# Kernel tuning notes

Hardware: AMD Instinct MI355X
Metric: run time of the kernel (lower is better)

The kernel has to match this reference:

```python
import jax, jax.numpy as jnp
import numpy as np

F, H, S, B, T = 1024, 512, 512, 32, 128  # feat_size, hid_size, seq_len, batch, max_out_len


def setup_inputs() -> dict:
    key = jax.random.key(0)
    ks = jax.random.split(key, 20)
    sc = 0.05
    def p(k, shape):
        return jax.random.normal(k, shape, dtype=jnp.float32) * sc
    return {
        "feats": jax.random.normal(ks[0], (S, B, F), dtype=jnp.float32),
        # encoder forward-direction LSTM (PyTorch gate order i,f,g,o)
        "Wih_f": p(ks[1], (4 * H, F)), "Whh_f": p(ks[2], (4 * H, H)),
        "bih_f": p(ks[3], (4 * H,)), "bhh_f": p(ks[4], (4 * H,)),
        # encoder backward-direction LSTM
        "Wih_b": p(ks[5], (4 * H, F)), "Whh_b": p(ks[6], (4 * H, H)),
        "bih_b": p(ks[7], (4 * H,)), "bhh_b": p(ks[8], (4 * H,)),
        # decoder LSTMCell(F -> 2H)
        "Wih_d": p(ks[9], (8 * H, F)), "Whh_d": p(ks[10], (8 * H, 2 * H)),
        "bih_d": p(ks[11], (8 * H,)), "bhh_d": p(ks[12], (8 * H,)),
        # attention projections
        "W_enc": p(ks[13], (H, 2 * H)), "b_enc": p(ks[14], (H,)),
        "W_dec": p(ks[15], (H, 2 * H)), "b_dec": p(ks[16], (H,)),
        "W_v": p(ks[17], (1, H)), "b_v": p(ks[18], (1,)),
    }


def _cell(x, h, c, Wih, Whh, bih, bhh):
    g = x @ Wih.T + h @ Whh.T + bih + bhh
    i, f, gg, o = jnp.split(g, 4, axis=-1)
    c = jax.nn.sigmoid(f) * c + jax.nn.sigmoid(i) * jnp.tanh(gg)
    return jax.nn.sigmoid(o) * jnp.tanh(c), c


def _run_lstm(seq, Wih, Whh, bih, bhh, hid):
    b = seq.shape[1]
    init = (jnp.zeros((b, hid), seq.dtype), jnp.zeros((b, hid), seq.dtype))
    def step(carry, x):
        h, c = _cell(x, carry[0], carry[1], Wih, Whh, bih, bhh)
        return (h, c), h
    (h, c), hs = jax.lax.scan(step, init, seq)
    return hs, h, c


def reference(feats, Wih_f, Whh_f, bih_f, bhh_f, Wih_b, Whh_b, bih_b, bhh_b,
              Wih_d, Whh_d, bih_d, bhh_d, W_enc, b_enc, W_dec, b_dec, W_v, b_v):
    s, b, _ = feats.shape
    hs_f, hf, cf = _run_lstm(feats, Wih_f, Whh_f, bih_f, bhh_f, H)
    hs_b, hb, cb = _run_lstm(feats[::-1], Wih_b, Whh_b, bih_b, bhh_b, H)
    enc_out = jnp.concatenate([hs_f, hs_b[::-1]], axis=-1)  # [S,B,2H]
    # torch h.view((B, -1)) on [2,B,H] is a raw reshape, reproduced exactly
    h0 = jnp.stack([hf, hb]).reshape(b, 2 * H)
    c0 = jnp.stack([cf, cb]).reshape(b, 2 * H)
    enc_proj = enc_out @ W_enc.T + b_enc  # [S,B,H], hoisted out of the step loop
    bidx = jnp.arange(b)

    def dec_step(carry, _):
        h, c, inp = carry
        h, c = _cell(inp, h, c, Wih_d, Whh_d, bih_d, bhh_d)
        dproj = h @ W_dec.T + b_dec  # [B,H]
        scores = (jnp.tanh(enc_proj + dproj[None]) @ W_v.T + b_v)[..., 0].T  # [B,S]
        idx = jnp.argmax(scores, axis=1)  # greedy pointer (is_train=False path)
        nxt = feats[idx, bidx]  # [B,F]
        return (h, c, nxt), scores

    _, ys = jax.lax.scan(dec_step, (h0, c0, feats[0]), None, length=T)  # [T,B,S]
    return ys.reshape(T * b, s)
```

## Files before the change

kernel.cpp:

```cpp
#include <hip/hip_runtime.h>
#include <stdint.h>


#define NWG 256

__device__ __forceinline__ float sigm(float x) { return 1.0f / (1.0f + __expf(-x)); }
__device__ __forceinline__ float tanhx(float x) {
  float e = __expf(2.0f * x);
  return 1.0f - 2.0f / (e + 1.0f);
}

__device__ __forceinline__ float ldc(const float* p) {
  return __hip_atomic_load(p, __ATOMIC_RELAXED, __HIP_MEMORY_SCOPE_AGENT);
}
__device__ __forceinline__ float2 ldc2(const float* p) {
  double d = __hip_atomic_load((const double*)p, __ATOMIC_RELAXED, __HIP_MEMORY_SCOPE_AGENT);
  return __builtin_bit_cast(float2, d);
}
__device__ __forceinline__ void stc(float* p, float v) {
  __hip_atomic_store(p, v, __ATOMIC_RELAXED, __HIP_MEMORY_SCOPE_AGENT);
}
__device__ __forceinline__ int ldci(const int* p) {
  return __hip_atomic_load(p, __ATOMIC_RELAXED, __HIP_MEMORY_SCOPE_AGENT);
}
__device__ __forceinline__ void stci(int* p, int v) {
  __hip_atomic_store(p, v, __ATOMIC_RELAXED, __HIP_MEMORY_SCOPE_AGENT);
}

__device__ __forceinline__ void tree_barrier(int* bar, int w, int epoch) {
  __syncthreads();
  if (threadIdx.x == 0) {
    const int g = w >> 3;
    int* gc = bar + g * 64;
    int* rc = bar + 2048;
    int* gf = bar + 2112 + g * 64;
    int old = __hip_atomic_fetch_add(gc, 1, __ATOMIC_RELAXED, __HIP_MEMORY_SCOPE_AGENT);
    if (old == epoch * 8 - 1) {
      __hip_atomic_fetch_add(rc, 1, __ATOMIC_RELAXED, __HIP_MEMORY_SCOPE_AGENT);
      while (__hip_atomic_load(rc, __ATOMIC_RELAXED, __HIP_MEMORY_SCOPE_AGENT) < epoch * 32)
        __builtin_amdgcn_s_sleep(2);
      __hip_atomic_store(gf, epoch, __ATOMIC_RELAXED, __HIP_MEMORY_SCOPE_AGENT);
    } else {
      while (__hip_atomic_load(gf, __ATOMIC_RELAXED, __HIP_MEMORY_SCOPE_AGENT) < epoch)
        __builtin_amdgcn_s_sleep(2);
    }
  }
  __syncthreads();
}

__global__ __launch_bounds__(256) void xproj_gemm(
    const float* __restrict__ A, const float* __restrict__ W,
    float* __restrict__ C)
{
  __shared__ float As[16][68];
  __shared__ float Ws[16][68];
  const int t = threadIdx.x;
  const int m0 = blockIdx.x * 64, n0 = blockIdx.y * 64;
  const int tx = t & 15, ty = t >> 4;
  const int lr = t >> 2, lk = (t & 3) * 4;
  float acc[4][4] = {{0.f}};

  for (int kb = 0; kb < 1024; kb += 16) {
    float4 a4 = *(const float4*)(A + (size_t)(m0 + lr) * 1024 + kb + lk);
    float4 w4 = *(const float4*)(W + (size_t)(n0 + lr) * 1024 + kb + lk);
    __syncthreads();
    As[lk + 0][lr] = a4.x; As[lk + 1][lr] = a4.y;
    As[lk + 2][lr] = a4.z; As[lk + 3][lr] = a4.w;
    Ws[lk + 0][lr] = w4.x; Ws[lk + 1][lr] = w4.y;
    Ws[lk + 2][lr] = w4.z; Ws[lk + 3][lr] = w4.w;
    __syncthreads();
#pragma unroll
    for (int kk = 0; kk < 16; ++kk) {
      float4 av = *(const float4*)(&As[kk][ty * 4]);
      float4 wv = *(const float4*)(&Ws[kk][tx * 4]);
      acc[0][0] += av.x * wv.x; acc[0][1] += av.x * wv.y;
      acc[0][2] += av.x * wv.z; acc[0][3] += av.x * wv.w;
      acc[1][0] += av.y * wv.x; acc[1][1] += av.y * wv.y;
      acc[1][2] += av.y * wv.z; acc[1][3] += av.y * wv.w;
      acc[2][0] += av.z * wv.x; acc[2][1] += av.z * wv.y;
      acc[2][2] += av.z * wv.z; acc[2][3] += av.z * wv.w;
      acc[3][0] += av.w * wv.x; acc[3][1] += av.w * wv.y;
      acc[3][2] += av.w * wv.z; acc[3][3] += av.w * wv.w;
    }
  }
#pragma unroll
  for (int i = 0; i < 4; ++i) {
    float4 o;
    o.x = acc[i][0]; o.y = acc[i][1]; o.z = acc[i][2]; o.w = acc[i][3];
    *(float4*)(C + (size_t)(m0 + ty * 4 + i) * 2048 + n0 + tx * 4) = o;
  }
}

__global__ __launch_bounds__(512) void encoder_kernel(
    const float* __restrict__ feats,
    const float* __restrict__ Wih_f, const float* __restrict__ Whh_f,
    const float* __restrict__ bih_f, const float* __restrict__ bhh_f,
    const float* __restrict__ Wih_b, const float* __restrict__ Whh_b,
    const float* __restrict__ bih_b, const float* __restrict__ bhh_b,
    const float* __restrict__ W_enc, const float* __restrict__ b_enc,
    const float* __restrict__ xg_f, const float* __restrict__ xg_b,
    float* __restrict__ enc_proj, float* __restrict__ henc,
    float* __restrict__ cfin, int* __restrict__ bar)
{
  extern __shared__ __align__(16) float dyn[];
  float* wih_l = dyn;
  float* whh_l = dyn + 16448;
  __shared__ float hch[32 * 132];
  __shared__ float wenc[4 * 516];
  __shared__ float gpart[32][17];
  __shared__ float projp[2][128];
  __shared__ float bias_s[16];
  __shared__ float benc_s[4];

  const int w = blockIdx.x;
  const int dir = (w >= 128) ? 1 : 0;
  const int wl = w & 127;
  const int col0 = wl * 4;
  const int t = threadIdx.x;
  const int g = t >> 7;
  const int tt = t & 127;
  const int b = tt >> 2;
  const int ci = tt & 3;
  const int col = col0 + ci;
  const int i0 = t, i1 = t + 512;
  const int bb0 = i0 >> 5, q0 = i0 & 31;
  const int bb1 = i1 >> 5, q1 = i1 & 31;

  const float* Wih = dir ? Wih_b : Wih_f;
  const float* Whh = dir ? Whh_b : Whh_f;
  const float* bih = dir ? bih_b : bih_f;
  const float* bhh = dir ? bhh_b : bhh_f;
  const float* xg  = dir ? xg_b : xg_f;

  if (!xg) {
    for (int i = t; i < 16 * 256; i += 512) {
      int r = i >> 8, q = i & 255;
      int gg = r >> 2, cj = r & 3;
      *(float4*)(wih_l + r * 1028 + q * 4) =
          *(const float4*)(Wih + (size_t)(gg * 512 + col0 + cj) * 1024 + q * 4);
    }
  }
  for (int i = t; i < 16 * 128; i += 512) {
    int r = i >> 7, q = i & 127;
    int gg = r >> 2, cj = r & 3;
    *(float4*)(whh_l + r * 516 + q * 4) =
        *(const float4*)(Whh + (size_t)(gg * 512 + col0 + cj) * 512 + q * 4);
  }
  for (int i = t; i < 4 * 128; i += 512) {
    int jl = i >> 7, q = i & 127;
    *(float4*)(wenc + jl * 516 + q * 4) =
        *(const float4*)(W_enc + (size_t)(col0 + jl) * 1024 + dir * 512 + q * 4);
  }
  if (t < 16) {
    int gg = t >> 2, cj = t & 3;
    bias_s[t] = bih[gg * 512 + col0 + cj] + bhh[gg * 512 + col0 + cj];
  }
  if (t < 4) benc_s[t] = b_enc[col0 + t];
  float c_reg = 0.0f;
  __syncthreads();

  const float* wx = wih_l + (g * 4 + ci) * 1028;
  const float* wh = whh_l + (g * 4 + ci) * 516;
  const float* wpe = wenc + ci * 516;
  const size_t xg_row = (size_t)(g * 512 + col);

  for (int it = 0; it < 512; ++it) {
    const int s = dir ? (511 - it) : it;
    float acc = 0.0f, projacc = 0.0f;
    float xgv = 0.0f;
    if (xg) xgv = xg[(size_t)(s * 32 + b) * 2048 + xg_row];

    if (it > 0) {
      const float* hsrc = henc + dir * 32768 + ((it - 1) & 1) * 16384;
      float2 rA0, rA1, rB0, rB1;
      rA0 = ldc2(hsrc + bb0 * 512 + q0 * 4);
      rA1 = ldc2(hsrc + bb0 * 512 + q0 * 4 + 2);
      rB0 = ldc2(hsrc + bb1 * 512 + q1 * 4);
      rB1 = ldc2(hsrc + bb1 * 512 + q1 * 4 + 2);
      for (int ch = 0; ch < 4; ++ch) {
        *(float4*)(hch + bb0 * 132 + q0 * 4) = make_float4(rA0.x, rA0.y, rA1.x, rA1.y);
        *(float4*)(hch + bb1 * 132 + q1 * 4) = make_float4(rB0.x, rB0.y, rB1.x, rB1.y);
        __syncthreads();
        if (ch < 3) {
          rA0 = ldc2(hsrc + bb0 * 512 + (ch + 1) * 128 + q0 * 4);
          rA1 = ldc2(hsrc + bb0 * 512 + (ch + 1) * 128 + q0 * 4 + 2);
          rB0 = ldc2(hsrc + bb1 * 512 + (ch + 1) * 128 + q1 * 4);
          rB1 = ldc2(hsrc + bb1 * 512 + (ch + 1) * 128 + q1 * 4 + 2);
        }
        {
          const float* hrow = hch + b * 132;
          const float* p0 = wh + ch * 128;
#pragma unroll 8
          for (int q = 0; q < 32; ++q) {
            float4 h4 = *(const float4*)(hrow + q * 4);
            float4 a4 = *(const float4*)(p0 + q * 4);
            acc += h4.x * a4.x + h4.y * a4.y + h4.z * a4.z + h4.w * a4.w;
          }
        }
        if (g < 2) {
          const float* hp = hch + b * 132 + g * 64;
          const float* wp = wpe + ch * 128 + g * 64;
#pragma unroll 4
          for (int kk = 0; kk < 16; ++kk) {
            float4 h4 = *(const float4*)(hp + kk * 4);
            float4 w4 = *(const float4*)(wp + kk * 4);
            projacc += h4.x * w4.x + h4.y * w4.y + h4.z * w4.z + h4.w * w4.w;
          }
        }
        __syncthreads();
      }
    }

    if (!xg) {
      const float* fsrc = feats + ((size_t)s * 32) * 1024;
      float4 fA = *(const float4*)(fsrc + bb0 * 1024 + q0 * 4);
      float4 fB = *(const float4*)(fsrc + bb1 * 1024 + q1 * 4);
      for (int ch = 0; ch < 8; ++ch) {
        *(float4*)(hch + bb0 * 132 + q0 * 4) = fA;
        *(float4*)(hch + bb1 * 132 + q1 * 4) = fB;
        __syncthreads();
        if (ch < 7) {
          fA = *(const float4*)(fsrc + bb0 * 1024 + (ch + 1) * 128 + q0 * 4);
          fB = *(const float4*)(fsrc + bb1 * 1024 + (ch + 1) * 128 + q1 * 4);
        }
        const float* hrow = hch + b * 132;
        const float* p0 = wx + ch * 128;
#pragma unroll 8
        for (int q = 0; q < 32; ++q) {
          float4 f4 = *(const float4*)(hrow + q * 4);
          float4 a4 = *(const float4*)(p0 + q * 4);
          acc += f4.x * a4.x + f4.y * a4.y + f4.z * a4.z + f4.w * a4.w;
        }
        __syncthreads();
      }
    }

    gpart[b][g * 4 + ci] = acc + xgv;
    if (g < 2) projp[g][tt] = projacc;
    __syncthreads();
    if (t < 128) {
      float gi = gpart[b][ci + 0] + bias_s[ci + 0];
      float gf = gpart[b][ci + 4] + bias_s[ci + 4];
      float gg = gpart[b][ci + 8] + bias_s[ci + 8];
      float go = gpart[b][ci + 12] + bias_s[ci + 12];
      float cn = sigm(gf) * c_reg + sigm(gi) * tanhx(gg);
      c_reg = cn;
      stc(henc + dir * 32768 + (it & 1) * 16384 + b * 512 + col,
          sigm(go) * tanhx(cn));
    } else if (g == 1 && it > 0) {
      const int sp = dir ? (512 - it) : (it - 1);
      const float p = projp[0][tt] + projp[1][tt];
      float* addr = enc_proj + ((size_t)sp * 32 + b) * 512 + col;
      if (it - 1 <= 255) {
        stc(addr, p + benc_s[ci]);
      } else {
        stc(addr, ldc(addr) + p);
      }
    }
    tree_barrier(bar, w, it + 1);
  }

  {
    const float* hsrc = henc + dir * 32768 + 16384;
    float projacc = 0.0f;
    for (int ch = 0; ch < 4; ++ch) {
      for (int i = t; i < 1024; i += 512) {
        int bb = i >> 5, q = i & 31;
        const float* sp = hsrc + bb * 512 + ch * 128 + q * 4;
        float2 f0 = ldc2(sp);
        float2 f1 = ldc2(sp + 2);
        *(float4*)(hch + bb * 132 + q * 4) = make_float4(f0.x, f0.y, f1.x, f1.y);
      }
      __syncthreads();
      if (g < 2) {
        const float* hp = hch + b * 132 + g * 64;
        const float* wp = wpe + ch * 128 + g * 64;
#pragma unroll 4
        for (int kk = 0; kk < 16; ++kk) {
          float4 h4 = *(const float4*)(hp + kk * 4);
          float4 w4 = *(const float4*)(wp + kk * 4);
          projacc += h4.x * w4.x + h4.y * w4.y + h4.z * w4.z + h4.w * w4.w;
        }
      }
      __syncthreads();
    }
    if (g < 2) projp[g][tt] = projacc;
    __syncthreads();
    if (g == 1) {
      const int sp = dir ? 0 : 511;
      float* addr = enc_proj + ((size_t)sp * 32 + b) * 512 + col;
      stc(addr, ldc(addr) + (projp[0][tt] + projp[1][tt]));
    }
    if (t < 128) cfin[dir * 16384 + b * 512 + col] = c_reg;
  }
}

__global__ __launch_bounds__(512) void decoder_kernel(
    const float* __restrict__ feats,
    const float* __restrict__ Wih_d, const float* __restrict__ Whh_d,
    const float* __restrict__ bih_d, const float* __restrict__ bhh_d,
    const float* __restrict__ W_dec, const float* __restrict__ b_dec,
    const float* __restrict__ W_v, const float* __restrict__ b_v,
    const float* __restrict__ enc_proj, const float* __restrict__ henc,
    const float* __restrict__ cfin,
    float* __restrict__ hbuf, float* __restrict__ dproj,
    float* __restrict__ pval, int* __restrict__ pidx,
    int* __restrict__ bar, float* __restrict__ out)
{
  extern __shared__ __align__(16) float dyn[];
  float* whh_l = dyn;
  float* wih_l = dyn + 16448;
  __shared__ float hch[32 * 132];
  __shared__ float gpart[2][32][17];
  __shared__ float c_lds[32][4];
  __shared__ float bias_s[16];
  __shared__ float svals[64];
  __shared__ int ib_lds[32];
  float* dpl = hch + 1088;

  const int w = blockIdx.x;
  const int t = threadIdx.x;
  const int q4 = t >> 7;
  const int tt = t & 127;
  const int b = tt >> 2;
  const int ci = tt & 3;
  const int col0 = w * 4;
  const int col = col0 + ci;
  const int i0 = t, i1 = t + 512;
  const int bb0 = i0 >> 5, q0 = i0 & 31;
  const int bb1 = i1 >> 5, q1 = i1 & 31;
  const int bb_c = w >> 3;
  const int qq_ = w & 7;
  const int ccB = t >> 8;
  const int bB = (t >> 3) & 31;
  const int k8 = t & 7;

  for (int i = t; i < 16 * 256; i += 512) {
    int r = i >> 8, q = i & 255;
    int gg = r >> 2, cj = r & 3;
    *(float4*)(whh_l + r * 1028 + q * 4) =
        *(const float4*)(Whh_d + (size_t)(gg * 1024 + col0 + cj) * 1024 + q * 4);
    *(float4*)(wih_l + r * 1028 + q * 4) =
        *(const float4*)(Wih_d + (size_t)(gg * 1024 + col0 + cj) * 1024 + q * 4);
  }
  if (t < 16) {
    int gg = t >> 2, cj = t & 3;
    bias_s[t] = bih_d[gg * 1024 + col0 + cj] + bhh_d[gg * 1024 + col0 + cj];
  }
  if (t < 128) {
    int flat = b * 1024 + col;
    int d = flat >> 14, sb = (flat >> 9) & 31, sh = flat & 511;
    float h0, c0;
    if (d == 0) {
      h0 = henc[16384 + sb * 512 + sh];
      c0 = cfin[sb * 512 + sh];
    } else {
      h0 = henc[32768 + 16384 + sb * 512 + sh];
      c0 = cfin[16384 + sb * 512 + sh];
    }
    stc(hbuf + b * 1024 + col, h0);
    c_lds[b][ci] = c0;
  }
  int bars = 1;
  tree_barrier(bar, w, bars);

  const float* wbase = (q4 < 2) ? whh_l : wih_l;
  const int g0 = (q4 & 1) * 2;
  const float* wr0 = wbase + (size_t)((g0 + 0) * 4 + ci) * 1028;
  const float* wr1 = wbase + (size_t)((g0 + 1) * 4 + ci) * 1028;

  for (int ts = 0; ts < 128; ++ts) {
    const float* hprev = hbuf + (ts & 1) * 32768;
    float* hnext = hbuf + ((ts + 1) & 1) * 32768;

    float a0 = 0.f, a1 = 0.f;
    const float* xrow = nullptr;
    {
      float2 rA0 = ldc2(hprev + bb0 * 1024 + q0 * 4);
      float2 rA1 = ldc2(hprev + bb0 * 1024 + q0 * 4 + 2);
      float2 rB0 = ldc2(hprev + bb1 * 1024 + q1 * 4);
      float2 rB1 = ldc2(hprev + bb1 * 1024 + q1 * 4 + 2);
      if (t < 32) {
        int ib = 0;
        if (ts > 0) {
          float v = ldc(pval + t * 8 + 0);
          int si = ldci(pidx + t * 8 + 0);
#pragma unroll
          for (int j = 1; j < 8; ++j) {
            float ov = ldc(pval + t * 8 + j);
            int os = ldci(pidx + t * 8 + j);
            if (ov > v || (ov == v && os < si)) { v = ov; si = os; }
          }
          ib = si;
        }
        ib_lds[t] = ib;
      }
      for (int ch = 0; ch < 8; ++ch) {
        *(float4*)(hch + bb0 * 132 + q0 * 4) = make_float4(rA0.x, rA0.y, rA1.x, rA1.y);
        *(float4*)(hch + bb1 * 132 + q1 * 4) = make_float4(rB0.x, rB0.y, rB1.x, rB1.y);
        __syncthreads();
        if (ch == 0 && q4 >= 2) {
          int ib = ib_lds[b];
          xrow = feats + ((size_t)ib * 32 + b) * 1024;
        }
        if (ch < 7) {
          rA0 = ldc2(hprev + bb0 * 1024 + (ch + 1) * 128 + q0 * 4);
          rA1 = ldc2(hprev + bb0 * 1024 + (ch + 1) * 128 + q0 * 4 + 2);
          rB0 = ldc2(hprev + bb1 * 1024 + (ch + 1) * 128 + q1 * 4);
          rB1 = ldc2(hprev + bb1 * 1024 + (ch + 1) * 128 + q1 * 4 + 2);
        }
        const float* src = (q4 < 2) ? (hch + b * 132) : (xrow + ch * 128);
        const float* p0 = wr0 + ch * 128;
        const float* p1 = wr1 + ch * 128;
#pragma unroll 8
        for (int qq = 0; qq < 32; ++qq) {
          float4 h4 = *(const float4*)(src + qq * 4);
          float4 u0 = *(const float4*)(p0 + qq * 4);
          float4 u1 = *(const float4*)(p1 + qq * 4);
          a0 += h4.x * u0.x + h4.y * u0.y + h4.z * u0.z + h4.w * u0.w;
          a1 += h4.x * u1.x + h4.y * u1.y + h4.z * u1.z + h4.w * u1.w;
        }
        __syncthreads();
      }
    }
    gpart[q4 >> 1][b][ci + (g0 + 0) * 4] = a0;
    gpart[q4 >> 1][b][ci + (g0 + 1) * 4] = a1;
    __syncthreads();
    if (t < 128) {
      float gi = gpart[0][b][ci + 0] + gpart[1][b][ci + 0] + bias_s[ci + 0];
      float gf = gpart[0][b][ci + 4] + gpart[1][b][ci + 4] + bias_s[ci + 4];
      float gg = gpart[0][b][ci + 8] + gpart[1][b][ci + 8] + bias_s[ci + 8];
      float go = gpart[0][b][ci + 12] + gpart[1][b][ci + 12] + bias_s[ci + 12];
      float cn = sigm(gf) * c_lds[b][ci] + sigm(gi) * tanhx(gg);
      c_lds[b][ci] = cn;
      stc(hnext + b * 1024 + col, sigm(go) * tanhx(cn));
    }
    ++bars; tree_barrier(bar, w, bars);

    {
      float dacc = 0.f;
      const float* wdrow = W_dec + (size_t)(2 * w + ccB) * 1024;
      float2 rA0 = ldc2(hnext + bb0 * 1024 + q0 * 4);
      float2 rA1 = ldc2(hnext + bb0 * 1024 + q0 * 4 + 2);
      float2 rB0 = ldc2(hnext + bb1 * 1024 + q1 * 4);
      float2 rB1 = ldc2(hnext + bb1 * 1024 + q1 * 4 + 2);
      for (int ch = 0; ch < 8; ++ch) {
        *(float4*)(hch + bb0 * 132 + q0 * 4) = make_float4(rA0.x, rA0.y, rA1.x, rA1.y);
        *(float4*)(hch + bb1 * 132 + q1 * 4) = make_float4(rB0.x, rB0.y, rB1.x, rB1.y);
        __syncthreads();
        if (ch < 7) {
          rA0 = ldc2(hnext + bb0 * 1024 + (ch + 1) * 128 + q0 * 4);
          rA1 = ldc2(hnext + bb0 * 1024 + (ch + 1) * 128 + q0 * 4 + 2);
          rB0 = ldc2(hnext + bb1 * 1024 + (ch + 1) * 128 + q1 * 4);
          rB1 = ldc2(hnext + bb1 * 1024 + (ch + 1) * 128 + q1 * 4 + 2);
        }
        const float* hl = hch + bB * 132 + k8 * 16;
        const float* wl = wdrow + ch * 128 + k8 * 16;
#pragma unroll
        for (int j = 0; j < 4; ++j) {
          float4 h4 = *(const float4*)(hl + j * 4);
          float4 w4 = *(const float4*)(wl + j * 4);
          dacc += h4.x * w4.x + h4.y * w4.y + h4.z * w4.z + h4.w * w4.w;
        }
        __syncthreads();
      }
      dacc += __shfl_xor(dacc, 1);
      dacc += __shfl_xor(dacc, 2);
      dacc += __shfl_xor(dacc, 4);
      if (k8 == 0) stc(dproj + bB * 512 + 2 * w + ccB, dacc + b_dec[2 * w + ccB]);
    }
    ++bars; tree_barrier(bar, w, bars);

    if (t < 256) {
      float2 v = ldc2(dproj + bb_c * 512 + 2 * t);
      int k = 2 * t;
      dpl[(k >> 6) * 68 + (k & 63) + 0] = v.x;
      dpl[(k >> 6) * 68 + (k & 63) + 1] = v.y;
    }
    __syncthreads();
    {
      const int sl = t >> 3, ks = t & 7;
      const int s = qq_ * 64 + sl;
      const float* ep = enc_proj + ((size_t)s * 32 + bb_c) * 512 + ks * 64;
      const float* dpp = dpl + ks * 68;
      const float* wvp = W_v + ks * 64;
      float sum = 0.f;
#pragma unroll 4
      for (int j = 0; j < 16; ++j) {
        float4 e4 = *(const float4*)(ep + j * 4);
        float4 d4 = *(const float4*)(dpp + j * 4);
        float4 v4 = *(const float4*)(wvp + j * 4);
        sum += tanhx(e4.x + d4.x) * v4.x;
        sum += tanhx(e4.y + d4.y) * v4.y;
        sum += tanhx(e4.z + d4.z) * v4.z;
        sum += tanhx(e4.w + d4.w) * v4.w;
      }
      sum += __shfl_xor(sum, 1);
      sum += __shfl_xor(sum, 2);
      sum += __shfl_xor(sum, 4);
      if (ks == 0) {
        float sv = sum + b_v[0];
        out[((size_t)ts * 32 + bb_c) * 512 + s] = sv;
        svals[sl] = sv;
      }
    }
    __syncthreads();
    if (t < 64) {
      float v = svals[t];
      int si = qq_ * 64 + t;
#pragma unroll
      for (int m = 1; m < 64; m <<= 1) {
        float ov = __shfl_xor(v, m);
        int os = __shfl_xor(si, m);
        if (ov > v || (ov == v && os < si)) { v = ov; si = os; }
      }
      if (t == 0) {
        stc(pval + bb_c * 8 + qq_, v);
        stci(pidx + bb_c * 8 + qq_, si);
      }
    }
    ++bars; tree_barrier(bar, w, bars);
  }
}

extern "C" void kernel_launch(void* const* d_in, const int* in_sizes, int n_in,
                              void* d_out, int out_size, void* d_ws, size_t ws_size,
                              hipStream_t stream) {
  (void)in_sizes; (void)n_in; (void)out_size;
  const float* feats = (const float*)d_in[0];
  const float* Wih_f = (const float*)d_in[1];
  const float* Whh_f = (const float*)d_in[2];
  const float* bih_f = (const float*)d_in[3];
  const float* bhh_f = (const float*)d_in[4];
  const float* Wih_b = (const float*)d_in[5];
  const float* Whh_b = (const float*)d_in[6];
  const float* bih_b = (const float*)d_in[7];
  const float* bhh_b = (const float*)d_in[8];
  const float* Wih_d = (const float*)d_in[9];
  const float* Whh_d = (const float*)d_in[10];
  const float* bih_d = (const float*)d_in[11];
  const float* bhh_d = (const float*)d_in[12];
  const float* W_enc = (const float*)d_in[13];
  const float* b_enc = (const float*)d_in[14];
  const float* W_dec = (const float*)d_in[15];
  const float* b_dec = (const float*)d_in[16];
  const float* W_v   = (const float*)d_in[17];
  const float* b_v   = (const float*)d_in[18];
  float* out = (float*)d_out;

  int* ctrl = (int*)d_ws;
  int* bar_enc = ctrl;
  int* bar_dec = ctrl + 8192;
  float* base = (float*)d_ws + 16384;
  float* enc_proj = base;
  float* henc     = enc_proj + 8388608;
  float* cfin     = henc + 65536;
  float* hbuf     = cfin + 32768;
  float* dproj    = hbuf + 65536;
  float* pval     = dproj + 16384;
  int*   pidx     = (int*)(pval + 8192);
  float* xg_base  = pval + 16384;

  const size_t xg_elems = (size_t)16384 * 2048;
  const size_t need_xg_bytes =
      (size_t)(16384 + 8388608 + 65536 + 32768 + 65536 + 16384 + 16384) * 4 +
      2 * xg_elems * 4 + (1 << 20);
  const bool use_xg = ws_size >= need_xg_bytes;
  const float* xg_f = use_xg ? xg_base : nullptr;
  const float* xg_b = use_xg ? (xg_base + xg_elems) : nullptr;

  const int ENC_LDS = (16 * 1028 + 16 * 516) * 4;
  const int DEC_LDS = (2 * 16 * 1028) * 4;
  hipFuncSetAttribute((const void*)encoder_kernel,
                      hipFuncAttributeMaxDynamicSharedMemorySize, ENC_LDS);
  hipFuncSetAttribute((const void*)decoder_kernel,
                      hipFuncAttributeMaxDynamicSharedMemorySize, DEC_LDS);

  hipMemsetAsync(d_ws, 0, 65536, stream);

  if (use_xg) {
    dim3 gg(256, 32);
    xproj_gemm<<<gg, 256, 0, stream>>>(feats, Wih_f, (float*)xg_f);
    xproj_gemm<<<gg, 256, 0, stream>>>(feats, Wih_b, (float*)xg_b);
  }

  {
    void* args[] = {(void*)&feats,
                    (void*)&Wih_f, (void*)&Whh_f, (void*)&bih_f, (void*)&bhh_f,
                    (void*)&Wih_b, (void*)&Whh_b, (void*)&bih_b, (void*)&bhh_b,
                    (void*)&W_enc, (void*)&b_enc, (void*)&xg_f, (void*)&xg_b,
                    (void*)&enc_proj, (void*)&henc, (void*)&cfin, (void*)&bar_enc};
    hipLaunchCooperativeKernel((const void*)encoder_kernel, dim3(NWG), dim3(512),
                               args, ENC_LDS, stream);
  }
  {
    void* args[] = {(void*)&feats,
                    (void*)&Wih_d, (void*)&Whh_d, (void*)&bih_d, (void*)&bhh_d,
                    (void*)&W_dec, (void*)&b_dec, (void*)&W_v, (void*)&b_v,
                    (void*)&enc_proj, (void*)&henc, (void*)&cfin,
                    (void*)&hbuf, (void*)&dproj, (void*)&pval, (void*)&pidx,
                    (void*)&bar_dec, (void*)&out};
    hipLaunchCooperativeKernel((const void*)decoder_kernel, dim3(NWG), dim3(512),
                               args, DEC_LDS, stream);
  }
}
```

Measured before the change: 19.38 ms.

## Drop precomputed input-projection GEMM and fuse x-projection into encoder recurrence

```diff
diff --git a/kernel.cpp b/kernel.cpp
--- a/kernel.cpp
+++ b/kernel.cpp
@@ -48,49 +48,6 @@
   __syncthreads();
 }
 
-__global__ __launch_bounds__(256) void xproj_gemm(
-    const float* __restrict__ A, const float* __restrict__ W,
-    float* __restrict__ C)
-{
-  __shared__ float As[16][68];
-  __shared__ float Ws[16][68];
-  const int t = threadIdx.x;
-  const int m0 = blockIdx.x * 64, n0 = blockIdx.y * 64;
-  const int tx = t & 15, ty = t >> 4;
-  const int lr = t >> 2, lk = (t & 3) * 4;
-  float acc[4][4] = {{0.f}};
-
-  for (int kb = 0; kb < 1024; kb += 16) {
-    float4 a4 = *(const float4*)(A + (size_t)(m0 + lr) * 1024 + kb + lk);
-    float4 w4 = *(const float4*)(W + (size_t)(n0 + lr) * 1024 + kb + lk);
-    __syncthreads();
-    As[lk + 0][lr] = a4.x; As[lk + 1][lr] = a4.y;
-    As[lk + 2][lr] = a4.z; As[lk + 3][lr] = a4.w;
-    Ws[lk + 0][lr] = w4.x; Ws[lk + 1][lr] = w4.y;
-    Ws[lk + 2][lr] = w4.z; Ws[lk + 3][lr] = w4.w;
-    __syncthreads();
-#pragma unroll
-    for (int kk = 0; kk < 16; ++kk) {
-      float4 av = *(const float4*)(&As[kk][ty * 4]);
-      float4 wv = *(const float4*)(&Ws[kk][tx * 4]);
-      acc[0][0] += av.x * wv.x; acc[0][1] += av.x * wv.y;
-      acc[0][2] += av.x * wv.z; acc[0][3] += av.x * wv.w;
-      acc[1][0] += av.y * wv.x; acc[1][1] += av.y * wv.y;
-      acc[1][2] += av.y * wv.z; acc[1][3] += av.y * wv.w;
-      acc[2][0] += av.z * wv.x; acc[2][1] += av.z * wv.y;
-      acc[2][2] += av.z * wv.z; acc[2][3] += av.z * wv.w;
-      acc[3][0] += av.w * wv.x; acc[3][1] += av.w * wv.y;
-      acc[3][2] += av.w * wv.z; acc[3][3] += av.w * wv.w;
-    }
-  }
-#pragma unroll
-  for (int i = 0; i < 4; ++i) {
-    float4 o;
-    o.x = acc[i][0]; o.y = acc[i][1]; o.z = acc[i][2]; o.w = acc[i][3];
-    *(float4*)(C + (size_t)(m0 + ty * 4 + i) * 2048 + n0 + tx * 4) = o;
-  }
-}
-
 __global__ __launch_bounds__(512) void encoder_kernel(
     const float* __restrict__ feats,
     const float* __restrict__ Wih_f, const float* __restrict__ Whh_f,
@@ -98,14 +55,13 @@
     const float* __restrict__ Wih_b, const float* __restrict__ Whh_b,
     const float* __restrict__ bih_b, const float* __restrict__ bhh_b,
     const float* __restrict__ W_enc, const float* __restrict__ b_enc,
-    const float* __restrict__ xg_f, const float* __restrict__ xg_b,
     float* __restrict__ enc_proj, float* __restrict__ henc,
     float* __restrict__ cfin, int* __restrict__ bar)
 {
   extern __shared__ __align__(16) float dyn[];
   float* wih_l = dyn;
   float* whh_l = dyn + 16448;
-  __shared__ float hch[32 * 132];
+  __shared__ float hch[32 * 260];
   __shared__ float wenc[4 * 516];
   __shared__ float gpart[32][17];
   __shared__ float projp[2][128];
@@ -122,23 +78,21 @@
   const int b = tt >> 2;
   const int ci = tt & 3;
   const int col = col0 + ci;
-  const int i0 = t, i1 = t + 512;
-  const int bb0 = i0 >> 5, q0 = i0 & 31;
-  const int bb1 = i1 >> 5, q1 = i1 & 31;
+  const int p0i = t,        p0b = p0i >> 6, p0q = p0i & 63;
+  const int p1i = t + 512,  p1b = p1i >> 6, p1q = p1i & 63;
+  const int p2i = t + 1024, p2b = p2i >> 6, p2q = p2i & 63;
+  const int p3i = t + 1536, p3b = p3i >> 6, p3q = p3i & 63;
 
   const float* Wih = dir ? Wih_b : Wih_f;
   const float* Whh = dir ? Whh_b : Whh_f;
   const float* bih = dir ? bih_b : bih_f;
   const float* bhh = dir ? bhh_b : bhh_f;
-  const float* xg  = dir ? xg_b : xg_f;
-
-  if (!xg) {
-    for (int i = t; i < 16 * 256; i += 512) {
-      int r = i >> 8, q = i & 255;
-      int gg = r >> 2, cj = r & 3;
-      *(float4*)(wih_l + r * 1028 + q * 4) =
-          *(const float4*)(Wih + (size_t)(gg * 512 + col0 + cj) * 1024 + q * 4);
-    }
+
+  for (int i = t; i < 16 * 256; i += 512) {
+    int r = i >> 8, q = i & 255;
+    int gg = r >> 2, cj = r & 3;
+    *(float4*)(wih_l + r * 1028 + q * 4) =
+        *(const float4*)(Wih + (size_t)(gg * 512 + col0 + cj) * 1024 + q * 4);
   }
   for (int i = t; i < 16 * 128; i += 512) {
     int r = i >> 7, q = i & 127;
@@ -162,80 +116,112 @@
   const float* wx = wih_l + (g * 4 + ci) * 1028;
   const float* wh = whh_l + (g * 4 + ci) * 516;
   const float* wpe = wenc + ci * 516;
-  const size_t xg_row = (size_t)(g * 512 + col);
 
   for (int it = 0; it < 512; ++it) {
     const int s = dir ? (511 - it) : it;
     float acc = 0.0f, projacc = 0.0f;
-    float xgv = 0.0f;
-    if (xg) xgv = xg[(size_t)(s * 32 + b) * 2048 + xg_row];
-
+    const float* fsrc = feats + ((size_t)s * 32) * 1024;
+    const float* hsrc = henc + dir * 32768 + ((it - 1) & 1) * 16384;
+
+    float2 h00a, h00b, h01a, h01b, h02a, h02b, h03a, h03b;
+    float2 h10a, h10b, h11a, h11b, h12a, h12b, h13a, h13b;
     if (it > 0) {
-      const float* hsrc = henc + dir * 32768 + ((it - 1) & 1) * 16384;
-      float2 rA0, rA1, rB0, rB1;
-      rA0 = ldc2(hsrc + bb0 * 512 + q0 * 4);
-      rA1 = ldc2(hsrc + bb0 * 512 + q0 * 4 + 2);
-      rB0 = ldc2(hsrc + bb1 * 512 + q1 * 4);
-      rB1 = ldc2(hsrc + bb1 * 512 + q1 * 4 + 2);
+      const float* sp;
+      sp = hsrc + p0b * 512 + p0q * 4;       h00a = ldc2(sp); h00b = ldc2(sp + 2);
+      sp = hsrc + p1b * 512 + p1q * 4;       h01a = ldc2(sp); h01b = ldc2(sp + 2);
+      sp = hsrc + p2b * 512 + p2q * 4;       h02a = ldc2(sp); h02b = ldc2(sp + 2);
+      sp = hsrc + p3b * 512 + p3q * 4;       h03a = ldc2(sp); h03b = ldc2(sp + 2);
+      sp = hsrc + p0b * 512 + 256 + p0q * 4; h10a = ldc2(sp); h10b = ldc2(sp + 2);
+      sp = hsrc + p1b * 512 + 256 + p1q * 4; h11a = ldc2(sp); h11b = ldc2(sp + 2);
+      sp = hsrc + p2b * 512 + 256 + p2q * 4; h12a = ldc2(sp); h12b = ldc2(sp + 2);
+      sp = hsrc + p3b * 512 + 256 + p3q * 4; h13a = ldc2(sp); h13b = ldc2(sp + 2);
+    }
+
+    {
+      float4 xv0 = *(const float4*)(fsrc + p0b * 1024 + p0q * 4);
+      float4 xv1 = *(const float4*)(fsrc + p1b * 1024 + p1q * 4);
+      float4 xv2 = *(const float4*)(fsrc + p2b * 1024 + p2q * 4);
+      float4 xv3 = *(const float4*)(fsrc + p3b * 1024 + p3q * 4);
       for (int ch = 0; ch < 4; ++ch) {
-        *(float4*)(hch + bb0 * 132 + q0 * 4) = make_float4(rA0.x, rA0.y, rA1.x, rA1.y);
-        *(float4*)(hch + bb1 * 132 + q1 * 4) = make_float4(rB0.x, rB0.y, rB1.x, rB1.y);
+        *(float4*)(hch + p0b * 260 + p0q * 4) = xv0;
+        *(float4*)(hch + p1b * 260 + p1q * 4) = xv1;
+        *(float4*)(hch + p2b * 260 + p2q * 4) = xv2;
+        *(float4*)(hch + p3b * 260 + p3q * 4) = xv3;
         __syncthreads();
         if (ch < 3) {
-          rA0 = ldc2(hsrc + bb0 * 512 + (ch + 1) * 128 + q0 * 4);
-          rA1 = ldc2(hsrc + bb0 * 512 + (ch + 1) * 128 + q0 * 4 + 2);
-          rB0 = ldc2(hsrc + bb1 * 512 + (ch + 1) * 128 + q1 * 4);
-          rB1 = ldc2(hsrc + bb1 * 512 + (ch + 1) * 128 + q1 * 4 + 2);
-        }
-        {
-          const float* hrow = hch + b * 132;
-          const float* p0 = wh + ch * 128;
+          xv0 = *(const float4*)(fsrc + p0b * 1024 + (ch + 1) * 256 + p0q * 4);
+          xv1 = *(const float4*)(fsrc + p1b * 1024 + (ch + 1) * 256 + p1q * 4);
+          xv2 = *(const float4*)(fsrc + p2b * 1024 + (ch + 1) * 256 + p2q * 4);
+          xv3 = *(const float4*)(fsrc + p3b * 1024 + (ch + 1) * 256 + p3q * 4);
+        }
+        const float* hrow = hch + b * 260;
+        const float* pw = wx + ch * 256;
 #pragma unroll 8
-          for (int q = 0; q < 32; ++q) {
-            float4 h4 = *(const float4*)(hrow + q * 4);
-            float4 a4 = *(const float4*)(p0 + q * 4);
-            acc += h4.x * a4.x + h4.y * a4.y + h4.z * a4.z + h4.w * a4.w;
-          }
+        for (int q = 0; q < 64; ++q) {
+          float4 f4 = *(const float4*)(hrow + q * 4);
+          float4 a4 = *(const float4*)(pw + q * 4);
+          acc += f4.x * a4.x + f4.y * a4.y + f4.z * a4.z + f4.w * a4.w;
+        }
+        __syncthreads();
+      }
+    }
+
+    if (it > 0) {
+      *(float4*)(hch + p0b * 260 + p0q * 4) = make_float4(h00a.x, h00a.y, h00b.x, h00b.y);
+      *(float4*)(hch + p1b * 260 + p1q * 4) = make_float4(h01a.x, h01a.y, h01b.x, h01b.y);
+      *(float4*)(hch + p2b * 260 + p2q * 4) = make_float4(h02a.x, h02a.y, h02b.x, h02b.y);
+      *(float4*)(hch + p3b * 260 + p3q * 4) = make_float4(h03a.x, h03a.y, h03b.x, h03b.y);
+      __syncthreads();
+      {
+        const float* hrow = hch + b * 260;
+        const float* pw = wh;
+#pragma unroll 8
+        for (int q = 0; q < 64; ++q) {
+          float4 h4 = *(const float4*)(hrow + q * 4);
+          float4 a4 = *(const float4*)(pw + q * 4);
+          acc += h4.x * a4.x + h4.y * a4.y + h4.z * a4.z + h4.w * a4.w;
         }
         if (g < 2) {
-          const float* hp = hch + b * 132 + g * 64;
-          const float* wp = wpe + ch * 128 + g * 64;
+          const float* hp = hch + b * 260 + g * 128;
+          const float* wp = wpe + g * 128;
 #pragma unroll 4
-          for (int kk = 0; kk < 16; ++kk) {
+          for (int kk = 0; kk < 32; ++kk) {
             float4 h4 = *(const float4*)(hp + kk * 4);
             float4 w4 = *(const float4*)(wp + kk * 4);
             projacc += h4.x * w4.x + h4.y * w4.y + h4.z * w4.z + h4.w * w4.w;
           }
         }
-        __syncthreads();
-      }
-    }
-
-    if (!xg) {
-      const float* fsrc = feats + ((size_t)s * 32) * 1024;
-      float4 fA = *(const float4*)(fsrc + bb0 * 1024 + q0 * 4);
-      float4 fB = *(const float4*)(fsrc + bb1 * 1024 + q1 * 4);
-      for (int ch = 0; ch < 8; ++ch) {
-        *(float4*)(hch + bb0 * 132 + q0 * 4) = fA;
-        *(float4*)(hch + bb1 * 132 + q1 * 4) = fB;
-        __syncthreads();
-        if (ch < 7) {
-          fA = *(const float4*)(fsrc + bb0 * 1024 + (ch + 1) * 128 + q0 * 4);
-          fB = *(const float4*)(fsrc + bb1 * 1024 + (ch + 1) * 128 + q1 * 4);
-        }
-        const float* hrow = hch + b * 132;
-        const float* p0 = wx + ch * 128;
+      }
+      __syncthreads();
+      *(float4*)(hch + p0b * 260 + p0q * 4) = make_float4(h10a.x, h10a.y, h10b.x, h10b.y);
+      *(float4*)(hch + p1b * 260 + p1q * 4) = make_float4(h11a.x, h11a.y, h11b.x, h11b.y);
+      *(float4*)(hch + p2b * 260 + p2q * 4) = make_float4(h12a.x, h12a.y, h12b.x, h12b.y);
+      *(float4*)(hch + p3b * 260 + p3q * 4) = make_float4(h13a.x, h13a.y, h13b.x, h13b.y);
+      __syncthreads();
+      {
+        const float* hrow = hch + b * 260;
+        const float* pw = wh + 256;
 #pragma unroll 8
-        for (int q = 0; q < 32; ++q) {
-          float4 f4 = *(const float4*)(hrow + q * 4);
-          float4 a4 = *(const float4*)(p0 + q * 4);
-          acc += f4.x * a4.x + f4.y * a4.y + f4.z * a4.z + f4.w * a4.w;
-        }
-        __syncthreads();
-      }
-    }
-
-    gpart[b][g * 4 + ci] = acc + xgv;
+        for (int q = 0; q < 64; ++q) {
+          float4 h4 = *(const float4*)(hrow + q * 4);
+          float4 a4 = *(const float4*)(pw + q * 4);
+          acc += h4.x * a4.x + h4.y * a4.y + h4.z * a4.z + h4.w * a4.w;
+        }
+        if (g < 2) {
+          const float* hp = hch + b * 260 + g * 128;
+          const float* wp = wpe + 256 + g * 128;
+#pragma unroll 4
+          for (int kk = 0; kk < 32; ++kk) {
+            float4 h4 = *(const float4*)(hp + kk * 4);
+            float4 w4 = *(const float4*)(wp + kk * 4);
+            projacc += h4.x * w4.x + h4.y * w4.y + h4.z * w4.z + h4.w * w4.w;
+          }
+        }
+      }
+      __syncthreads();
+    }
+
+    gpart[b][g * 4 + ci] = acc;
     if (g < 2) projp[g][tt] = projacc;
     __syncthreads();
     if (t < 128) {
@@ -263,20 +249,20 @@
   {
     const float* hsrc = henc + dir * 32768 + 16384;
     float projacc = 0.0f;
-    for (int ch = 0; ch < 4; ++ch) {
-      for (int i = t; i < 1024; i += 512) {
-        int bb = i >> 5, q = i & 31;
-        const float* sp = hsrc + bb * 512 + ch * 128 + q * 4;
+    for (int ch = 0; ch < 2; ++ch) {
+      for (int i = t; i < 2048; i += 512) {
+        int bb = i >> 6, qf = i & 63;
+        const float* sp = hsrc + bb * 512 + ch * 256 + qf * 4;
         float2 f0 = ldc2(sp);
         float2 f1 = ldc2(sp + 2);
-        *(float4*)(hch + bb * 132 + q * 4) = make_float4(f0.x, f0.y, f1.x, f1.y);
+        *(float4*)(hch + bb * 260 + qf * 4) = make_float4(f0.x, f0.y, f1.x, f1.y);
       }
       __syncthreads();
       if (g < 2) {
-        const float* hp = hch + b * 132 + g * 64;
-        const float* wp = wpe + ch * 128 + g * 64;
+        const float* hp = hch + b * 260 + g * 128;
+        const float* wp = wpe + ch * 256 + g * 128;
 #pragma unroll 4
-        for (int kk = 0; kk < 16; ++kk) {
+        for (int kk = 0; kk < 32; ++kk) {
           float4 h4 = *(const float4*)(hp + kk * 4);
           float4 w4 = *(const float4*)(wp + kk * 4);
           projacc += h4.x * w4.x + h4.y * w4.y + h4.z * w4.z + h4.w * w4.w;
@@ -376,10 +362,14 @@
     float a0 = 0.f, a1 = 0.f;
     const float* xrow = nullptr;
     {
-      float2 rA0 = ldc2(hprev + bb0 * 1024 + q0 * 4);
-      float2 rA1 = ldc2(hprev + bb0 * 1024 + q0 * 4 + 2);
-      float2 rB0 = ldc2(hprev + bb1 * 1024 + q1 * 4);
-      float2 rB1 = ldc2(hprev + bb1 * 1024 + q1 * 4 + 2);
+      float2 s0a0 = ldc2(hprev + bb0 * 1024 + q0 * 4);
+      float2 s0a1 = ldc2(hprev + bb0 * 1024 + q0 * 4 + 2);
+      float2 s0b0 = ldc2(hprev + bb1 * 1024 + q1 * 4);
+      float2 s0b1 = ldc2(hprev + bb1 * 1024 + q1 * 4 + 2);
+      float2 s1a0 = ldc2(hprev + bb0 * 1024 + 128 + q0 * 4);
+      float2 s1a1 = ldc2(hprev + bb0 * 1024 + 128 + q0 * 4 + 2);
+      float2 s1b0 = ldc2(hprev + bb1 * 1024 + 128 + q1 * 4);
+      float2 s1b1 = ldc2(hprev + bb1 * 1024 + 128 + q1 * 4 + 2);
       if (t < 32) {
         int ib = 0;
         if (ts > 0) {
@@ -396,18 +386,31 @@
         ib_lds[t] = ib;
       }
       for (int ch = 0; ch < 8; ++ch) {
-        *(float4*)(hch + bb0 * 132 + q0 * 4) = make_float4(rA0.x, rA0.y, rA1.x, rA1.y);
-        *(float4*)(hch + bb1 * 132 + q1 * 4) = make_float4(rB0.x, rB0.y, rB1.x, rB1.y);
+        if (ch & 1) {
+          *(float4*)(hch + bb0 * 132 + q0 * 4) = make_float4(s1a0.x, s1a0.y, s1a1.x, s1a1.y);
+          *(float4*)(hch + bb1 * 132 + q1 * 4) = make_float4(s1b0.x, s1b0.y, s1b1.x, s1b1.y);
+        } else {
+          *(float4*)(hch + bb0 * 132 + q0 * 4) = make_float4(s0a0.x, s0a0.y, s0a1.x, s0a1.y);
+          *(float4*)(hch + bb1 * 132 + q1 * 4) = make_float4(s0b0.x, s0b0.y, s0b1.x, s0b1.y);
+        }
         __syncthreads();
         if (ch == 0 && q4 >= 2) {
           int ib = ib_lds[b];
           xrow = feats + ((size_t)ib * 32 + b) * 1024;
         }
-        if (ch < 7) {
-          rA0 = ldc2(hprev + bb0 * 1024 + (ch + 1) * 128 + q0 * 4);
-          rA1 = ldc2(hprev + bb0 * 1024 + (ch + 1) * 128 + q0 * 4 + 2);
-          rB0 = ldc2(hprev + bb1 * 1024 + (ch + 1) * 128 + q1 * 4);
-          rB1 = ldc2(hprev + bb1 * 1024 + (ch + 1) * 128 + q1 * 4 + 2);
+        if (ch < 6) {
+          const int cn = (ch + 2) * 128;
+          if (ch & 1) {
+            s1a0 = ldc2(hprev + bb0 * 1024 + cn + q0 * 4);
+            s1a1 = ldc2(hprev + bb0 * 1024 + cn + q0 * 4 + 2);
+            s1b0 = ldc2(hprev + bb1 * 1024 + cn + q1 * 4);
+            s1b1 = ldc2(hprev + bb1 * 1024 + cn + q1 * 4 + 2);
+          } else {
+            s0a0 = ldc2(hprev + bb0 * 1024 + cn + q0 * 4);
+            s0a1 = ldc2(hprev + bb0 * 1024 + cn + q0 * 4 + 2);
+            s0b0 = ldc2(hprev + bb1 * 1024 + cn + q1 * 4);
+            s0b1 = ldc2(hprev + bb1 * 1024 + cn + q1 * 4 + 2);
+          }
         }
         const float* src = (q4 < 2) ? (hch + b * 132) : (xrow + ch * 128);
         const float* p0 = wr0 + ch * 128;
@@ -440,19 +443,36 @@
     {
       float dacc = 0.f;
       const float* wdrow = W_dec + (size_t)(2 * w + ccB) * 1024;
-      float2 rA0 = ldc2(hnext + bb0 * 1024 + q0 * 4);
-      float2 rA1 = ldc2(hnext + bb0 * 1024 + q0 * 4 + 2);
-      float2 rB0 = ldc2(hnext + bb1 * 1024 + q1 * 4);
-      float2 rB1 = ldc2(hnext + bb1 * 1024 + q1 * 4 + 2);
+      float2 s0a0 = ldc2(hnext + bb0 * 1024 + q0 * 4);
+      float2 s0a1 = ldc2(hnext + bb0 * 1024 + q0 * 4 + 2);
+      float2 s0b0 = ldc2(hnext + bb1 * 1024 + q1 * 4);
+      float2 s0b1 = ldc2(hnext + bb1 * 1024 + q1 * 4 + 2);
+      float2 s1a0 = ldc2(hnext + bb0 * 1024 + 128 + q0 * 4);
+      float2 s1a1 = ldc2(hnext + bb0 * 1024 + 128 + q0 * 4 + 2);
+      float2 s1b0 = ldc2(hnext + bb1 * 1024 + 128 + q1 * 4);
+      float2 s1b1 = ldc2(hnext + bb1 * 1024 + 128 + q1 * 4 + 2);
       for (int ch = 0; ch < 8; ++ch) {
-        *(float4*)(hch + bb0 * 132 + q0 * 4) = make_float4(rA0.x, rA0.y, rA1.x, rA1.y);
-        *(float4*)(hch + bb1 * 132 + q1 * 4) = make_float4(rB0.x, rB0.y, rB1.x, rB1.y);
+        if (ch & 1) {
+          *(float4*)(hch + bb0 * 132 + q0 * 4) = make_float4(s1a0.x, s1a0.y, s1a1.x, s1a1.y);
+          *(float4*)(hch + bb1 * 132 + q1 * 4) = make_float4(s1b0.x, s1b0.y, s1b1.x, s1b1.y);
+        } else {
+          *(float4*)(hch + bb0 * 132 + q0 * 4) = make_float4(s0a0.x, s0a0.y, s0a1.x, s0a1.y);
+          *(float4*)(hch + bb1 * 132 + q1 * 4) = make_float4(s0b0.x, s0b0.y, s0b1.x, s0b1.y);
+        }
         __syncthreads();
-        if (ch < 7) {
-          rA0 = ldc2(hnext + bb0 * 1024 + (ch + 1) * 128 + q0 * 4);
-          rA1 = ldc2(hnext + bb0 * 1024 + (ch + 1) * 128 + q0 * 4 + 2);
-          rB0 = ldc2(hnext + bb1 * 1024 + (ch + 1) * 128 + q1 * 4);
-          rB1 = ldc2(hnext + bb1 * 1024 + (ch + 1) * 128 + q1 * 4 + 2);
+        if (ch < 6) {
+          const int cn = (ch + 2) * 128;
+          if (ch & 1) {
+            s1a0 = ldc2(hnext + bb0 * 1024 + cn + q0 * 4);
+            s1a1 = ldc2(hnext + bb0 * 1024 + cn + q0 * 4 + 2);
+            s1b0 = ldc2(hnext + bb1 * 1024 + cn + q1 * 4);
+            s1b1 = ldc2(hnext + bb1 * 1024 + cn + q1 * 4 + 2);
+          } else {
+            s0a0 = ldc2(hnext + bb0 * 1024 + cn + q0 * 4);
+            s0a1 = ldc2(hnext + bb0 * 1024 + cn + q0 * 4 + 2);
+            s0b0 = ldc2(hnext + bb1 * 1024 + cn + q1 * 4);
+            s0b1 = ldc2(hnext + bb1 * 1024 + cn + q1 * 4 + 2);
+          }
         }
         const float* hl = hch + bB * 132 + k8 * 16;
         const float* wl = wdrow + ch * 128 + k8 * 16;
@@ -526,7 +546,7 @@
 extern "C" void kernel_launch(void* const* d_in, const int* in_sizes, int n_in,
                               void* d_out, int out_size, void* d_ws, size_t ws_size,
                               hipStream_t stream) {
-  (void)in_sizes; (void)n_in; (void)out_size;
+  (void)in_sizes; (void)n_in; (void)out_size; (void)ws_size;
   const float* feats = (const float*)d_in[0];
   const float* Wih_f = (const float*)d_in[1];
   const float* Whh_f = (const float*)d_in[2];
@@ -559,15 +579,6 @@
   float* dproj    = hbuf + 65536;
   float* pval     = dproj + 16384;
   int*   pidx     = (int*)(pval + 8192);
-  float* xg_base  = pval + 16384;
-
-  const size_t xg_elems = (size_t)16384 * 2048;
-  const size_t need_xg_bytes =
-      (size_t)(16384 + 8388608 + 65536 + 32768 + 65536 + 16384 + 16384) * 4 +
-      2 * xg_elems * 4 + (1 << 20);
-  const bool use_xg = ws_size >= need_xg_bytes;
-  const float* xg_f = use_xg ? xg_base : nullptr;
-  const float* xg_b = use_xg ? (xg_base + xg_elems) : nullptr;
 
   const int ENC_LDS = (16 * 1028 + 16 * 516) * 4;
   const int DEC_LDS = (2 * 16 * 1028) * 4;
@@ -578,17 +589,11 @@
 
   hipMemsetAsync(d_ws, 0, 65536, stream);
 
-  if (use_xg) {
-    dim3 gg(256, 32);
-    xproj_gemm<<<gg, 256, 0, stream>>>(feats, Wih_f, (float*)xg_f);
-    xproj_gemm<<<gg, 256, 0, stream>>>(feats, Wih_b, (float*)xg_b);
-  }
-
   {
     void* args[] = {(void*)&feats,
                     (void*)&Wih_f, (void*)&Whh_f, (void*)&bih_f, (void*)&bhh_f,
                     (void*)&Wih_b, (void*)&Whh_b, (void*)&bih_b, (void*)&bhh_b,
-                    (void*)&W_enc, (void*)&b_enc, (void*)&xg_f, (void*)&xg_b,
+                    (void*)&W_enc, (void*)&b_enc,
                     (void*)&enc_proj, (void*)&henc, (void*)&cfin, (void*)&bar_enc};
     hipLaunchCooperativeKernel((const void*)encoder_kernel, dim3(NWG), dim3(512),
                                args, ENC_LDS, stream);
```

Result: faster. 17.66 ms (-8.9%).
